# Kernel optimization log

Hardware: AMD Instinct MI355X
Metric: run time of the kernel (lower is better)

## Reference

```python
import jax, jax.numpy as jnp
import numpy as np

NUM_HEADS = 16
D_MODEL = 1024
D_QKV = 64


def _xavier(key, shape):
    # xavier normal over last two dims (fan_in = D_MODEL, fan_out = D_QKV)
    std = float(np.sqrt(2.0 / (shape[-2] + shape[-1])))
    return jax.random.normal(key, shape, dtype=jnp.float32) * std


def setup_inputs() -> dict:
    key = jax.random.key(0)
    ks = jax.random.split(key, 9)
    B, L = 4, 2048
    q = jax.random.normal(ks[0], (B, L, D_MODEL), dtype=jnp.float32)
    k = jax.random.normal(ks[1], (B, L, D_MODEL), dtype=jnp.float32)
    v = jax.random.normal(ks[2], (B, L, D_MODEL), dtype=jnp.float32)
    mask = jax.random.randint(ks[3], (B, L, L), 0, 2, dtype=jnp.int32)
    Wq = _xavier(ks[4], (NUM_HEADS, D_MODEL, D_QKV))
    Wk = _xavier(ks[5], (NUM_HEADS, D_MODEL, D_QKV))
    Wv = _xavier(ks[6], (NUM_HEADS, D_MODEL, D_QKV))
    lim = float(1.0 / np.sqrt(D_MODEL))
    Wo_w = jax.random.uniform(ks[7], (D_MODEL, D_MODEL), minval=-lim, maxval=lim, dtype=jnp.float32)
    Wo_b = jax.random.uniform(ks[8], (D_MODEL,), minval=-lim, maxval=lim, dtype=jnp.float32)
    return {"q": q, "k": k, "v": v, "mask": mask,
            "Wq": Wq, "Wk": Wk, "Wv": Wv, "Wo_w": Wo_w, "Wo_b": Wo_b}


def reference(q, k, v, mask, Wq, Wk, Wv, Wo_w, Wo_b):
    B, L, _ = q.shape
    query = jnp.einsum('blm,nmd->bnld', q, Wq)   # [B,H,L,Dq]
    key_ = jnp.einsum('blm,nmd->bnld', k, Wk)
    value = jnp.einsum('blm,nmd->bnld', v, Wv)
    scores = jnp.einsum('bnld,bnmd->bnlm', query, key_) / jnp.sqrt(
        jnp.asarray(D_QKV, dtype=query.dtype))          # [B,H,L,L]
    scores = jnp.where(mask[:, None, :, :] == 0, jnp.asarray(-1e9, scores.dtype), scores)
    attn = jax.nn.softmax(scores, axis=-1)
    out = jnp.einsum('bnlm,bnmd->bnld', attn, value)     # [B,H,L,Dq]
    out = out.transpose(0, 2, 1, 3).reshape(B, L, D_MODEL)
    return out @ Wo_w.T + Wo_b
```

## Files before the change

kernel.cpp:

```cpp
#include <hip/hip_runtime.h>
#include <stdint.h>

typedef __bf16 bf16;
typedef __bf16 bf16x8 __attribute__((ext_vector_type(8)));
typedef float  f32x4  __attribute__((ext_vector_type(4)));
typedef uint32_t u32;
typedef uint64_t u64;

#define SCALE_L2E 0.18033688011112042f

__device__ __forceinline__ void gld_lds16(const void* gsrc, void* ldst) {
  __builtin_amdgcn_global_load_lds(
      (const __attribute__((address_space(1))) void*)gsrc,
      (__attribute__((address_space(3))) void*)ldst, 16, 0, 0);
}

__global__ void prep(const float* __restrict__ q, const float* __restrict__ k,
                     const float* __restrict__ v, const int* __restrict__ mask,
                     const float* __restrict__ Wq, const float* __restrict__ Wk,
                     const float* __restrict__ Wv, const float* __restrict__ Wo,
                     bf16* __restrict__ qkv, bf16* __restrict__ Wt, u32* __restrict__ mbits) {
  __shared__ float lds[64][65];
  const int z = blockIdx.z;
  const int t = threadIdx.x;
  const int tg = blockIdx.x * 256 + t;
  if (z < 3) {
    const float* in = (z == 0) ? q : (z == 1) ? k : v;
    bf16* o = qkv + (size_t)z * 8388608;
#pragma unroll
    for (int it = 0; it < 2; ++it) {
      int i = tg + it * 524288;
      const float4* p = (const float4*)(in + (size_t)i * 8);
      float4 a = p[0], b = p[1];
      bf16x8 vv;
      vv[0]=(bf16)a.x; vv[1]=(bf16)a.y; vv[2]=(bf16)a.z; vv[3]=(bf16)a.w;
      vv[4]=(bf16)b.x; vv[5]=(bf16)b.y; vv[6]=(bf16)b.z; vv[7]=(bf16)b.w;
      *(bf16x8*)(o + (size_t)i * 8) = vv;
    }
  } else if (z == 3) {
    const int blk = blockIdx.x;
    if (blk < 768) {
      int s = blk >> 8, sub = blk & 255;
      int h = sub >> 4, mblk = sub & 15;
      const float* W = (s == 0) ? Wq : (s == 1) ? Wk : Wv;
      const float* src = W + h * 65536 + mblk * 4096;
#pragma unroll
      for (int i = 0; i < 16; ++i) {
        int idx = t + i * 256;
        lds[idx >> 6][idx & 63] = src[idx];
      }
      __syncthreads();
      int d = t >> 2, o0 = t & 3;
#pragma unroll
      for (int oo = 0; oo < 2; ++oo) {
        int o = o0 + oo * 4;
        bf16x8 vv;
#pragma unroll
        for (int j = 0; j < 8; ++j)
          vv[j] = (bf16)lds[o * 8 + j][d];
        *(bf16x8*)&Wt[(size_t)s * 1048576 + (size_t)(h * 64 + d) * 1024 + mblk * 64 + o * 8] = vv;
      }
    } else if (blk < 832) {
      int idx0 = (blk - 768) * 256 + t;
      for (int i = idx0; i < 131072; i += 16384) {
        const float4* p = (const float4*)&Wo[i * 8];
        float4 a = p[0], b = p[1];
        bf16x8 vv;
        vv[0]=(bf16)a.x; vv[1]=(bf16)a.y; vv[2]=(bf16)a.z; vv[3]=(bf16)a.w;
        vv[4]=(bf16)b.x; vv[5]=(bf16)b.y; vv[6]=(bf16)b.z; vv[7]=(bf16)b.w;
        *(bf16x8*)&Wt[3145728 + (size_t)i * 8] = vv;
      }
    }
  } else {
    for (int idx = tg; idx < 16777216; idx += 524288) {
      int m = mask[idx];
      u64 bal = __ballot(m != 0);
      if ((t & 63) == 0)
        *(u64*)&mbits[idx >> 5] = bal;
    }
  }
}

#define GEMM_CORE(Ap_, Bp_)                                                    \
  __shared__ bf16 sA[2][4096];                                                 \
  __shared__ bf16 sB[2][4096];                                                 \
  const int tid = threadIdx.x;                                                 \
  const int lane = tid & 63, w = tid >> 6;                                     \
  const int c = lane & 15, g = lane >> 4;                                      \
  const int wr = w >> 1, wc = w & 1;                                           \
  const int rr0 = tid >> 3, p0 = tid & 7;                                      \
  const int l0 = p0 ^ (rr0 & 7);                                               \
  const size_t so0 = (size_t)(2 * rr0 + (l0 >> 2)) * 1024 + (l0 & 3) * 8;      \
  const int rr1 = (256 + tid) >> 3, p1 = tid & 7;                              \
  const int l1 = p1 ^ (rr1 & 7);                                               \
  const size_t so1 = (size_t)(2 * rr1 + (l1 >> 2)) * 1024 + (l1 & 3) * 8;      \
  const bf16* As0 = (Ap_) + so0;                                               \
  const bf16* As1 = (Ap_) + so1;                                               \
  const bf16* Bs0 = (Bp_) + so0;                                               \
  const bf16* Bs1 = (Bp_) + so1;                                               \
  const int fro = (c >> 1) * 128 + ((((c & 1) * 4 + g) ^ (c >> 1)) << 4);      \
  const int abase = wr * 4096 + fro;                                           \
  const int bbase = wc * 4096 + fro;                                           \
  f32x4 acc[4][4] = {};                                                        \
  gld_lds16(As0, (char*)&sA[0][0] + tid * 16);                                 \
  gld_lds16(As1, (char*)&sA[0][0] + 4096 + tid * 16);                          \
  gld_lds16(Bs0, (char*)&sB[0][0] + tid * 16);                                 \
  gld_lds16(Bs1, (char*)&sB[0][0] + 4096 + tid * 16);                          \
  for (int k0 = 0; k0 < 1024; k0 += 32) {                                      \
    __syncthreads();                                                           \
    int cb = (k0 >> 5) & 1, nb = cb ^ 1;                                       \
    if (k0 < 992) {                                                            \
      gld_lds16(As0 + k0 + 32, (char*)&sA[nb][0] + tid * 16);                  \
      gld_lds16(As1 + k0 + 32, (char*)&sA[nb][0] + 4096 + tid * 16);           \
      gld_lds16(Bs0 + k0 + 32, (char*)&sB[nb][0] + tid * 16);                  \
      gld_lds16(Bs1 + k0 + 32, (char*)&sB[nb][0] + 4096 + tid * 16);           \
    }                                                                          \
    const char* a8 = (const char*)&sA[cb][0] + abase;                          \
    const char* b8 = (const char*)&sB[cb][0] + bbase;                          \
    bf16x8 af[4], bfr[4];                                                      \
    _Pragma("unroll")                                                          \
    for (int m = 0; m < 4; ++m)                                                \
      af[m] = *(const bf16x8*)(a8 + m * 1024);                                 \
    _Pragma("unroll")                                                          \
    for (int n = 0; n < 4; ++n)                                                \
      bfr[n] = *(const bf16x8*)(b8 + n * 1024);                                \
    _Pragma("unroll")                                                          \
    for (int m = 0; m < 4; ++m)                                                \
      _Pragma("unroll")                                                        \
      for (int n = 0; n < 4; ++n)                                              \
        acc[m][n] = __builtin_amdgcn_mfma_f32_16x16x32_bf16(af[m], bfr[n], acc[m][n], 0, 0, 0); \
  }

__global__ __launch_bounds__(256, 4)
void proj_fused(const bf16* __restrict__ qkv, const bf16* __restrict__ Wt,
                bf16* __restrict__ Qp, bf16* __restrict__ Kp, bf16* __restrict__ Vt) {
  const int wg = blockIdx.x;
  const bf16* Ap;
  const bf16* Bp;
  int row0, col0, stage;
  if (wg < 1024) {
    int swz = (wg & 7) * 128 + (wg >> 3);
    int bx = swz & 7, by = swz >> 3;
    row0 = by * 128; col0 = bx * 128;
    stage = (row0 >= 8192) ? 1 : 0;
    Ap = qkv + (size_t)row0 * 1024;
    Bp = Wt + (stage ? 1048576 : 0) + (size_t)col0 * 1024;
  } else {
    int w2 = wg - 1024;
    int bz = w2 >> 7, rem = w2 & 127;
    int swz = (rem & 7) * 16 + (rem >> 3);
    int bx = swz & 15, by = swz >> 4;
    row0 = by * 128; col0 = bx * 128;
    stage = 2 + bz;
    Ap = Wt + 2097152 + (size_t)row0 * 1024;
    Bp = qkv + 16777216 + (size_t)bz * 2097152 + (size_t)col0 * 1024;
  }

  GEMM_CORE(Ap, Bp)

  if (stage <= 1) {
    float csc = stage ? 1.0f : SCALE_L2E;
    bf16* dst = stage ? Kp : Qp;
#pragma unroll
    for (int m = 0; m < 4; ++m) {
      int row_base = (row0 & 8191) + wr * 64 + m * 16 + g * 4;
#pragma unroll
      for (int n = 0; n < 4; ++n) {
        int col = col0 + wc * 64 + n * 16 + c;
#pragma unroll
        for (int r = 0; r < 4; ++r) {
          int row = row_base + r;
          int b = row >> 11, l = row & 2047, h = col >> 6, d = col & 63;
          dst[(((size_t)(b * 16 + h) * 2048 + l) << 6) + d] = (bf16)(acc[m][n][r] * csc);
        }
      }
    }
  } else {
    int bz = stage - 2;
#pragma unroll
    for (int m = 0; m < 4; ++m) {
      int row_base = row0 + wr * 64 + m * 16 + g * 4;
#pragma unroll
      for (int n = 0; n < 4; ++n) {
        int col = col0 + wc * 64 + n * 16 + c;
#pragma unroll
        for (int r = 0; r < 4; ++r)
          Vt[((size_t)(bz * 1024 + row_base + r)) * 2048 + col] = (bf16)acc[m][n][r];
      }
    }
  }
}

__global__ __launch_bounds__(256, 4)
void gemm_out(const bf16* __restrict__ X, const bf16* __restrict__ Wot,
              float* __restrict__ out, const float* __restrict__ bias) {
  int lin = blockIdx.y * 8 + blockIdx.x;
  int swz = (lin & 7) * 64 + (lin >> 3);
  int bx = swz & 7, by = swz >> 3;
  const int row0 = by * 128, col0 = bx * 128;
  const bf16* Ap = X + (size_t)row0 * 1024;
  const bf16* Bp = Wot + (size_t)col0 * 1024;

  GEMM_CORE(Ap, Bp)

#pragma unroll
  for (int m = 0; m < 4; ++m) {
    int row_base = row0 + wr * 64 + m * 16 + g * 4;
#pragma unroll
    for (int n = 0; n < 4; ++n) {
      int col = col0 + wc * 64 + n * 16 + c;
#pragma unroll
      for (int r = 0; r < 4; ++r)
        out[(size_t)(row_base + r) * 1024 + col] = acc[m][n][r] + bias[col];
    }
  }
}

__global__ __launch_bounds__(256, 4)
void attn_fwd(const bf16* __restrict__ Qp, const bf16* __restrict__ Kp,
              const bf16* __restrict__ Vt, const u32* __restrict__ mbits,
              bf16* __restrict__ X) {
  int lin = blockIdx.y * 16 + blockIdx.x;
  int swz = (lin & 7) * 128 + (lin >> 3);
  int qt = swz & 15, bh = swz >> 4;
  int b = bh >> 4, h = bh & 15;
  int q0 = qt * 128;

  const int tid = threadIdx.x;
  const int lane = tid & 63, w = tid >> 6;
  const int c = lane & 15, g = lane >> 4;

  __shared__ char smem[24576];
  char* sKV = smem;
  char* sPw = smem + 16384 + w * 2048;

  const int c7 = c & 7;
  const int ko0 = c * 128 + ((g ^ c7) << 4);
  const int ko1 = c * 128 + (((4 + g) ^ c7) << 4);
  const int pr_off = (c >> 1) * 128 + ((((c & 1) * 4 + g) ^ (c >> 1)) << 4);
  int pwo[2];
#pragma unroll
  for (int nk = 0; nk < 2; ++nk)
    pwo[nk] = (c >> 1) * 128 + ((((c & 1) * 4 + nk * 2 + (g >> 1)) ^ (c >> 1)) << 4) + (g & 1) * 8;

  const int kr_ = tid >> 3, kb_ = tid & 7;
  const int dK = kr_ * 128 + ((kb_ ^ (kr_ & 7)) << 4);
  const int vd_ = tid >> 2, vk_ = tid & 3;
  const int dV = 4096 + (vd_ >> 1) * 128 + (((((vd_ & 1) << 2) + vk_) ^ ((vd_ >> 1) & 7)) << 4);
  const bf16* gK = Kp + (size_t)bh * 131072 + kr_ * 64 + kb_ * 8;
  const bf16* gV = Vt + ((size_t)(b * 1024 + h * 64 + vd_)) * 2048 + vk_ * 8;

  const bf16* Qbase = Qp + ((size_t)bh * 2048) * 64;
  bf16x8 qf[2][2];
#pragma unroll
  for (int nq = 0; nq < 2; ++nq) {
    int qg = q0 + w * 32 + nq * 16 + c;
#pragma unroll
    for (int kk = 0; kk < 2; ++kk)
      qf[nq][kk] = *(const bf16x8*)&Qbase[(size_t)qg * 64 + kk * 32 + g * 8];
  }

  bf16x8 onesv;
#pragma unroll
  for (int i = 0; i < 8; ++i) onesv[i] = (bf16)1.0f;

  const u32* Mrow0 = mbits + ((size_t)b * 2048 + (q0 + w * 32 + c)) * 64;
  const u32* Mrow1 = mbits + ((size_t)b * 2048 + (q0 + w * 32 + 16 + c)) * 64;

  f32x4 oacc[4][2] = {};
  f32x4 dacc[2] = {};

  {
    uint4 kr = *(const uint4*)gK;
    uint4 vr = *(const uint4*)gV;
    *(uint4*)(sKV + dK) = kr;
    *(uint4*)(sKV + dV) = vr;
  }
  u32 mw0 = Mrow0[0], mw1 = Mrow1[0];

  for (int t = 0; t < 64; ++t) {
    __syncthreads();
    const char* kbuf = sKV + ((t & 1) << 13);

    uint4 kr, vr;
    u32 mn0 = 0, mn1 = 0;
    if (t < 63) {
      kr = *(const uint4*)(gK + (size_t)(t + 1) * 2048);
      vr = *(const uint4*)(gV + (size_t)(t + 1) * 32);
      mn0 = Mrow0[t + 1];
      mn1 = Mrow1[t + 1];
    }

    f32x4 st[2][2] = {};
    __builtin_amdgcn_s_setprio(1);
#pragma unroll
    for (int nk = 0; nk < 2; ++nk) {
      bf16x8 kfa = *(const bf16x8*)(kbuf + ko0 + nk * 2048);
      st[nk][0] = __builtin_amdgcn_mfma_f32_16x16x32_bf16(kfa, qf[0][0], st[nk][0], 0, 0, 0);
      st[nk][1] = __builtin_amdgcn_mfma_f32_16x16x32_bf16(kfa, qf[1][0], st[nk][1], 0, 0, 0);
      bf16x8 kfb = *(const bf16x8*)(kbuf + ko1 + nk * 2048);
      st[nk][0] = __builtin_amdgcn_mfma_f32_16x16x32_bf16(kfb, qf[0][1], st[nk][0], 0, 0, 0);
      st[nk][1] = __builtin_amdgcn_mfma_f32_16x16x32_bf16(kfb, qf[1][1], st[nk][1], 0, 0, 0);
    }
    __builtin_amdgcn_s_setprio(0);

#pragma unroll
    for (int nq = 0; nq < 2; ++nq) {
      u32 ms = (nq ? mw1 : mw0) >> (4 * g);
#pragma unroll
      for (int nk = 0; nk < 2; ++nk) {
        const int bs = nk * 16;
        float e0 = __builtin_amdgcn_exp2f(st[nk][nq][0]);
        float e1 = __builtin_amdgcn_exp2f(st[nk][nq][1]);
        float e2 = __builtin_amdgcn_exp2f(st[nk][nq][2]);
        float e3 = __builtin_amdgcn_exp2f(st[nk][nq][3]);
        e0 = (ms & (1u << (bs + 0))) ? e0 : 0.f;
        e1 = (ms & (1u << (bs + 1))) ? e1 : 0.f;
        e2 = (ms & (1u << (bs + 2))) ? e2 : 0.f;
        e3 = (ms & (1u << (bs + 3))) ? e3 : 0.f;
        union { bf16 hh[4]; uint2 dd; } pk;
        pk.hh[0] = (bf16)e0; pk.hh[1] = (bf16)e1;
        pk.hh[2] = (bf16)e2; pk.hh[3] = (bf16)e3;
        *(uint2*)(sPw + pwo[nk] + nq * 1024) = pk.dd;
      }
    }

    __builtin_amdgcn_s_setprio(1);
    {
      bf16x8 pf0 = *(const bf16x8*)(sPw + pr_off);
      bf16x8 pf1 = *(const bf16x8*)(sPw + pr_off + 1024);
      dacc[0] = __builtin_amdgcn_mfma_f32_16x16x32_bf16(onesv, pf0, dacc[0], 0, 0, 0);
      dacc[1] = __builtin_amdgcn_mfma_f32_16x16x32_bf16(onesv, pf1, dacc[1], 0, 0, 0);
#pragma unroll
      for (int md = 0; md < 4; ++md) {
        bf16x8 vf = *(const bf16x8*)(kbuf + 4096 + pr_off + md * 1024);
        oacc[md][0] = __builtin_amdgcn_mfma_f32_16x16x32_bf16(vf, pf0, oacc[md][0], 0, 0, 0);
        oacc[md][1] = __builtin_amdgcn_mfma_f32_16x16x32_bf16(vf, pf1, oacc[md][1], 0, 0, 0);
      }
    }
    __builtin_amdgcn_s_setprio(0);

    if (t < 63) {
      char* nbuf = sKV + (((t + 1) & 1) << 13);
      *(uint4*)(nbuf + dK) = kr;
      *(uint4*)(nbuf + dV) = vr;
    }
    mw0 = mn0; mw1 = mn1;
  }

  float inv0 = 1.f / dacc[0][0];
  float inv1 = 1.f / dacc[1][0];

  __syncthreads();
  char* Xl = smem;
#pragma unroll
  for (int nq = 0; nq < 2; ++nq) {
    float inv = nq ? inv1 : inv0;
    int ql = w * 32 + nq * 16 + c;
#pragma unroll
    for (int md = 0; md < 4; ++md)
#pragma unroll
      for (int r = 0; r < 4; ++r) {
        int d = md * 16 + g * 4 + r;
        int blk = d >> 3, off = d & 7;
        *(bf16*)(Xl + ql * 128 + ((blk ^ (ql & 7)) << 4) + off * 2) =
            (bf16)(oacc[md][nq][r] * inv);
      }
  }
  __syncthreads();
#pragma unroll
  for (int i = 0; i < 4; ++i) {
    int u = i * 256 + tid;
    int row = u >> 3, blk = u & 7;
    uint4 xv = *(const uint4*)(Xl + row * 128 + ((blk ^ (row & 7)) << 4));
    *(uint4*)&X[(size_t)(b * 2048 + q0 + row) * 1024 + h * 64 + blk * 8] = xv;
  }
}


extern "C" void kernel_launch(void* const* d_in, const int* in_sizes, int n_in,
                              void* d_out, int out_size, void* d_ws, size_t ws_size,
                              hipStream_t stream) {
  const float* q    = (const float*)d_in[0];
  const float* k    = (const float*)d_in[1];
  const float* v    = (const float*)d_in[2];
  const int*   mask = (const int*)d_in[3];
  const float* Wq   = (const float*)d_in[4];
  const float* Wk   = (const float*)d_in[5];
  const float* Wv   = (const float*)d_in[6];
  const float* Wo   = (const float*)d_in[7];
  const float* Wb   = (const float*)d_in[8];

  char* ws = (char*)d_ws;
  bf16* qkv = (bf16*)(ws + 0);
  bf16* Wt  = (bf16*)(ws + 50331648);
  bf16* Qp  = (bf16*)(ws + 58720256);
  bf16* Kp  = (bf16*)(ws + 75497472);
  bf16* Vt  = (bf16*)(ws + 92274688);
  bf16* Xb  = (bf16*)(ws + 109051904);
  u32*  mb  = (u32*) (ws + 125829120);

  prep<<<dim3(2048, 1, 5), 256, 0, stream>>>(q, k, v, mask, Wq, Wk, Wv, Wo, qkv, Wt, mb);

  proj_fused<<<dim3(1536, 1, 1), 256, 0, stream>>>(qkv, Wt, Qp, Kp, Vt);

  attn_fwd<<<dim3(16, 64, 1), 256, 0, stream>>>(Qp, Kp, Vt, mb, Xb);

  gemm_out<<<dim3(8, 64, 1), 256, 0, stream>>>(Xb, Wt + 3145728, (float*)d_out, Wb);
}
```

Measured before the change: 247.5 us.

## Fuse fp32-to-bf16 input conversion into projection GEMM tile loads

Drops the separate pass that converted q/k/v activations to a bf16 workspace. The projection GEMM now loads fp32 tiles straight into registers, converts them, and writes packed bf16 into LDS, with the write placed after the MFMA block as a register-staged prefetch. This saves a full fp32 read plus a bf16 write and re-read of 48M elements. In exchange the fused path reads fp32 tiles again per column tile (about 8x reuse) and loses the async global-to-LDS path for the fp32 operand, which adds register pressure. The prep kernel is also flattened and the bias load is hoisted out of the inner loop.

```diff
diff --git a/kernel.cpp b/kernel.cpp
--- a/kernel.cpp
+++ b/kernel.cpp
@@ -15,63 +15,53 @@
       (__attribute__((address_space(3))) void*)ldst, 16, 0, 0);
 }
 
-__global__ void prep(const float* __restrict__ q, const float* __restrict__ k,
-                     const float* __restrict__ v, const int* __restrict__ mask,
+__device__ __forceinline__ void pack_wr(float4 x0, float4 x1, void* dst) {
+  bf16x8 vv;
+  vv[0]=(bf16)x0.x; vv[1]=(bf16)x0.y; vv[2]=(bf16)x0.z; vv[3]=(bf16)x0.w;
+  vv[4]=(bf16)x1.x; vv[5]=(bf16)x1.y; vv[6]=(bf16)x1.z; vv[7]=(bf16)x1.w;
+  *(bf16x8*)dst = vv;
+}
+
+__global__ void prep(const int* __restrict__ mask,
                      const float* __restrict__ Wq, const float* __restrict__ Wk,
                      const float* __restrict__ Wv, const float* __restrict__ Wo,
-                     bf16* __restrict__ qkv, bf16* __restrict__ Wt, u32* __restrict__ mbits) {
+                     bf16* __restrict__ Wt, u32* __restrict__ mbits) {
   __shared__ float lds[64][65];
-  const int z = blockIdx.z;
+  const int blk = blockIdx.x;
   const int t = threadIdx.x;
-  const int tg = blockIdx.x * 256 + t;
-  if (z < 3) {
-    const float* in = (z == 0) ? q : (z == 1) ? k : v;
-    bf16* o = qkv + (size_t)z * 8388608;
-#pragma unroll
-    for (int it = 0; it < 2; ++it) {
-      int i = tg + it * 524288;
-      const float4* p = (const float4*)(in + (size_t)i * 8);
+  if (blk < 768) {
+    int s = blk >> 8, sub = blk & 255;
+    int h = sub >> 4, mblk = sub & 15;
+    const float* W = (s == 0) ? Wq : (s == 1) ? Wk : Wv;
+    const float* src = W + h * 65536 + mblk * 4096;
+#pragma unroll
+    for (int i = 0; i < 16; ++i) {
+      int idx = t + i * 256;
+      lds[idx >> 6][idx & 63] = src[idx];
+    }
+    __syncthreads();
+    int d = t >> 2, o0 = t & 3;
+#pragma unroll
+    for (int oo = 0; oo < 2; ++oo) {
+      int o = o0 + oo * 4;
+      bf16x8 vv;
+#pragma unroll
+      for (int j = 0; j < 8; ++j)
+        vv[j] = (bf16)lds[o * 8 + j][d];
+      *(bf16x8*)&Wt[(size_t)s * 1048576 + (size_t)(h * 64 + d) * 1024 + mblk * 64 + o * 8] = vv;
+    }
+  } else if (blk < 832) {
+    int idx0 = (blk - 768) * 256 + t;
+    for (int i = idx0; i < 131072; i += 16384) {
+      const float4* p = (const float4*)&Wo[i * 8];
       float4 a = p[0], b = p[1];
       bf16x8 vv;
       vv[0]=(bf16)a.x; vv[1]=(bf16)a.y; vv[2]=(bf16)a.z; vv[3]=(bf16)a.w;
       vv[4]=(bf16)b.x; vv[5]=(bf16)b.y; vv[6]=(bf16)b.z; vv[7]=(bf16)b.w;
-      *(bf16x8*)(o + (size_t)i * 8) = vv;
-    }
-  } else if (z == 3) {
-    const int blk = blockIdx.x;
-    if (blk < 768) {
-      int s = blk >> 8, sub = blk & 255;
-      int h = sub >> 4, mblk = sub & 15;
-      const float* W = (s == 0) ? Wq : (s == 1) ? Wk : Wv;
-      const float* src = W + h * 65536 + mblk * 4096;
-#pragma unroll
-      for (int i = 0; i < 16; ++i) {
-        int idx = t + i * 256;
-        lds[idx >> 6][idx & 63] = src[idx];
-      }
-      __syncthreads();
-      int d = t >> 2, o0 = t & 3;
-#pragma unroll
-      for (int oo = 0; oo < 2; ++oo) {
-        int o = o0 + oo * 4;
-        bf16x8 vv;
-#pragma unroll
-        for (int j = 0; j < 8; ++j)
-          vv[j] = (bf16)lds[o * 8 + j][d];
-        *(bf16x8*)&Wt[(size_t)s * 1048576 + (size_t)(h * 64 + d) * 1024 + mblk * 64 + o * 8] = vv;
-      }
-    } else if (blk < 832) {
-      int idx0 = (blk - 768) * 256 + t;
-      for (int i = idx0; i < 131072; i += 16384) {
-        const float4* p = (const float4*)&Wo[i * 8];
-        float4 a = p[0], b = p[1];
-        bf16x8 vv;
-        vv[0]=(bf16)a.x; vv[1]=(bf16)a.y; vv[2]=(bf16)a.z; vv[3]=(bf16)a.w;
-        vv[4]=(bf16)b.x; vv[5]=(bf16)b.y; vv[6]=(bf16)b.z; vv[7]=(bf16)b.w;
-        *(bf16x8*)&Wt[3145728 + (size_t)i * 8] = vv;
-      }
+      *(bf16x8*)&Wt[3145728 + (size_t)i * 8] = vv;
     }
   } else {
+    int tg = (blk - 832) * 256 + t;
     for (int idx = tg; idx < 16777216; idx += 524288) {
       int m = mask[idx];
       u64 bal = __ballot(m != 0);
@@ -81,102 +71,151 @@
   }
 }
 
-#define GEMM_CORE(Ap_, Bp_)                                                    \
-  __shared__ bf16 sA[2][4096];                                                 \
-  __shared__ bf16 sB[2][4096];                                                 \
-  const int tid = threadIdx.x;                                                 \
-  const int lane = tid & 63, w = tid >> 6;                                     \
-  const int c = lane & 15, g = lane >> 4;                                      \
-  const int wr = w >> 1, wc = w & 1;                                           \
-  const int rr0 = tid >> 3, p0 = tid & 7;                                      \
-  const int l0 = p0 ^ (rr0 & 7);                                               \
-  const size_t so0 = (size_t)(2 * rr0 + (l0 >> 2)) * 1024 + (l0 & 3) * 8;      \
-  const int rr1 = (256 + tid) >> 3, p1 = tid & 7;                              \
-  const int l1 = p1 ^ (rr1 & 7);                                               \
-  const size_t so1 = (size_t)(2 * rr1 + (l1 >> 2)) * 1024 + (l1 & 3) * 8;      \
-  const bf16* As0 = (Ap_) + so0;                                               \
-  const bf16* As1 = (Ap_) + so1;                                               \
-  const bf16* Bs0 = (Bp_) + so0;                                               \
-  const bf16* Bs1 = (Bp_) + so1;                                               \
-  const int fro = (c >> 1) * 128 + ((((c & 1) * 4 + g) ^ (c >> 1)) << 4);      \
-  const int abase = wr * 4096 + fro;                                           \
-  const int bbase = wc * 4096 + fro;                                           \
-  f32x4 acc[4][4] = {};                                                        \
-  gld_lds16(As0, (char*)&sA[0][0] + tid * 16);                                 \
-  gld_lds16(As1, (char*)&sA[0][0] + 4096 + tid * 16);                          \
-  gld_lds16(Bs0, (char*)&sB[0][0] + tid * 16);                                 \
-  gld_lds16(Bs1, (char*)&sB[0][0] + 4096 + tid * 16);                          \
-  for (int k0 = 0; k0 < 1024; k0 += 32) {                                      \
-    __syncthreads();                                                           \
-    int cb = (k0 >> 5) & 1, nb = cb ^ 1;                                       \
-    if (k0 < 992) {                                                            \
-      gld_lds16(As0 + k0 + 32, (char*)&sA[nb][0] + tid * 16);                  \
-      gld_lds16(As1 + k0 + 32, (char*)&sA[nb][0] + 4096 + tid * 16);           \
-      gld_lds16(Bs0 + k0 + 32, (char*)&sB[nb][0] + tid * 16);                  \
-      gld_lds16(Bs1 + k0 + 32, (char*)&sB[nb][0] + 4096 + tid * 16);           \
-    }                                                                          \
-    const char* a8 = (const char*)&sA[cb][0] + abase;                          \
-    const char* b8 = (const char*)&sB[cb][0] + bbase;                          \
-    bf16x8 af[4], bfr[4];                                                      \
-    _Pragma("unroll")                                                          \
-    for (int m = 0; m < 4; ++m)                                                \
-      af[m] = *(const bf16x8*)(a8 + m * 1024);                                 \
-    _Pragma("unroll")                                                          \
-    for (int n = 0; n < 4; ++n)                                                \
-      bfr[n] = *(const bf16x8*)(b8 + n * 1024);                                \
-    _Pragma("unroll")                                                          \
-    for (int m = 0; m < 4; ++m)                                                \
-      _Pragma("unroll")                                                        \
-      for (int n = 0; n < 4; ++n)                                              \
-        acc[m][n] = __builtin_amdgcn_mfma_f32_16x16x32_bf16(af[m], bfr[n], acc[m][n], 0, 0, 0); \
-  }
+template<bool AF, bool BF>
+__device__ __forceinline__ void gemm_core(
+    const float* Af, const bf16* Ab,
+    const float* Bf, const bf16* Bb,
+    bf16 (&sA)[2][4096], bf16 (&sB)[2][4096],
+    f32x4 (&acc)[4][4])
+{
+  const int tid = threadIdx.x;
+  const int lane = tid & 63, w = tid >> 6;
+  const int c = lane & 15, g = lane >> 4;
+  const int wr = w >> 1, wc = w & 1;
+
+  const int rr0 = tid >> 3;
+  const int l0 = (tid & 7) ^ (rr0 & 7);
+  const size_t soA0 = (size_t)(2 * rr0 + (l0 >> 2)) * 1024 + (l0 & 3) * 8;
+  const size_t soA1 = soA0 + (size_t)64 * 1024;
+
+  const int fro = (c >> 1) * 128 + ((((c & 1) * 4 + g) ^ (c >> 1)) << 4);
+  const int abase = wr * 4096 + fro;
+  const int bbase = wc * 4096 + fro;
+
+  char* dA0 = (char*)&sA[0][0];
+  char* dB0 = (char*)&sB[0][0];
+
+  if constexpr (AF) {
+    pack_wr(*(const float4*)(Af + soA0), *(const float4*)(Af + soA0 + 4), dA0 + tid * 16);
+    pack_wr(*(const float4*)(Af + soA1), *(const float4*)(Af + soA1 + 4), dA0 + 4096 + tid * 16);
+  } else {
+    gld_lds16(Ab + soA0, dA0 + tid * 16);
+    gld_lds16(Ab + soA1, dA0 + 4096 + tid * 16);
+  }
+  if constexpr (BF) {
+    pack_wr(*(const float4*)(Bf + soA0), *(const float4*)(Bf + soA0 + 4), dB0 + tid * 16);
+    pack_wr(*(const float4*)(Bf + soA1), *(const float4*)(Bf + soA1 + 4), dB0 + 4096 + tid * 16);
+  } else {
+    gld_lds16(Bb + soA0, dB0 + tid * 16);
+    gld_lds16(Bb + soA1, dB0 + 4096 + tid * 16);
+  }
+
+  for (int k0 = 0; k0 < 1024; k0 += 32) {
+    __syncthreads();
+    const int cb = (k0 >> 5) & 1, nb = cb ^ 1;
+    char* dAn = (char*)&sA[nb][0];
+    char* dBn = (char*)&sB[nb][0];
+
+    float4 ra0, ra1, ra2, ra3, rb0, rb1, rb2, rb3;
+    if (k0 < 992) {
+      if constexpr (AF) {
+        ra0 = *(const float4*)(Af + soA0 + k0 + 32);
+        ra1 = *(const float4*)(Af + soA0 + k0 + 36);
+        ra2 = *(const float4*)(Af + soA1 + k0 + 32);
+        ra3 = *(const float4*)(Af + soA1 + k0 + 36);
+      } else {
+        gld_lds16(Ab + soA0 + k0 + 32, dAn + tid * 16);
+        gld_lds16(Ab + soA1 + k0 + 32, dAn + 4096 + tid * 16);
+      }
+      if constexpr (BF) {
+        rb0 = *(const float4*)(Bf + soA0 + k0 + 32);
+        rb1 = *(const float4*)(Bf + soA0 + k0 + 36);
+        rb2 = *(const float4*)(Bf + soA1 + k0 + 32);
+        rb3 = *(const float4*)(Bf + soA1 + k0 + 36);
+      } else {
+        gld_lds16(Bb + soA0 + k0 + 32, dBn + tid * 16);
+        gld_lds16(Bb + soA1 + k0 + 32, dBn + 4096 + tid * 16);
+      }
+    }
+
+    const char* a8 = (const char*)&sA[cb][0] + abase;
+    const char* b8 = (const char*)&sB[cb][0] + bbase;
+    bf16x8 af[4], bfr[4];
+#pragma unroll
+    for (int m = 0; m < 4; ++m)
+      af[m] = *(const bf16x8*)(a8 + m * 1024);
+#pragma unroll
+    for (int n = 0; n < 4; ++n)
+      bfr[n] = *(const bf16x8*)(b8 + n * 1024);
+#pragma unroll
+    for (int m = 0; m < 4; ++m)
+#pragma unroll
+      for (int n = 0; n < 4; ++n)
+        acc[m][n] = __builtin_amdgcn_mfma_f32_16x16x32_bf16(af[m], bfr[n], acc[m][n], 0, 0, 0);
+
+    if (k0 < 992) {
+      if constexpr (AF) {
+        pack_wr(ra0, ra1, dAn + tid * 16);
+        pack_wr(ra2, ra3, dAn + 4096 + tid * 16);
+      }
+      if constexpr (BF) {
+        pack_wr(rb0, rb1, dBn + tid * 16);
+        pack_wr(rb2, rb3, dBn + 4096 + tid * 16);
+      }
+    }
+  }
+}
 
 __global__ __launch_bounds__(256, 4)
-void proj_fused(const bf16* __restrict__ qkv, const bf16* __restrict__ Wt,
+void proj_fused(const float* __restrict__ q, const float* __restrict__ k,
+                const float* __restrict__ v, const bf16* __restrict__ Wt,
                 bf16* __restrict__ Qp, bf16* __restrict__ Kp, bf16* __restrict__ Vt) {
+  __shared__ bf16 sA[2][4096];
+  __shared__ bf16 sB[2][4096];
   const int wg = blockIdx.x;
-  const bf16* Ap;
-  const bf16* Bp;
-  int row0, col0, stage;
+  const int lane = threadIdx.x & 63, w = threadIdx.x >> 6;
+  const int c = lane & 15, g = lane >> 4;
+  const int wr = w >> 1, wc = w & 1;
+  f32x4 acc[4][4] = {};
+
   if (wg < 1024) {
     int swz = (wg & 7) * 128 + (wg >> 3);
     int bx = swz & 7, by = swz >> 3;
-    row0 = by * 128; col0 = bx * 128;
-    stage = (row0 >= 8192) ? 1 : 0;
-    Ap = qkv + (size_t)row0 * 1024;
-    Bp = Wt + (stage ? 1048576 : 0) + (size_t)col0 * 1024;
+    const int row0 = by * 128, col0 = bx * 128;
+    const int isK = (row0 >= 8192);
+    const float* Af = isK ? (k + (size_t)(row0 - 8192) * 1024)
+                          : (q + (size_t)row0 * 1024);
+    const bf16* Bb = Wt + (isK ? 1048576 : 0) + (size_t)col0 * 1024;
+
+    gemm_core<true, false>(Af, nullptr, nullptr, Bb, sA, sB, acc);
+
+    float csc = isK ? 1.0f : SCALE_L2E;
+    bf16* dst = isK ? Kp : Qp;
+#pragma unroll
+    for (int m = 0; m < 4; ++m) {
+      int row_base = (row0 & 8191) + wr * 64 + m * 16 + g * 4;
+#pragma unroll
+      for (int n = 0; n < 4; ++n) {
+        int col = col0 + wc * 64 + n * 16 + c;
+#pragma unroll
+        for (int r = 0; r < 4; ++r) {
+          int row = row_base + r;
+          int b = row >> 11, l = row & 2047, h = col >> 6, d = col & 63;
+          dst[(((size_t)(b * 16 + h) * 2048 + l) << 6) + d] = (bf16)(acc[m][n][r] * csc);
+        }
+      }
+    }
   } else {
     int w2 = wg - 1024;
     int bz = w2 >> 7, rem = w2 & 127;
     int swz = (rem & 7) * 16 + (rem >> 3);
     int bx = swz & 15, by = swz >> 4;
-    row0 = by * 128; col0 = bx * 128;
-    stage = 2 + bz;
-    Ap = Wt + 2097152 + (size_t)row0 * 1024;
-    Bp = qkv + 16777216 + (size_t)bz * 2097152 + (size_t)col0 * 1024;
-  }
-
-  GEMM_CORE(Ap, Bp)
-
-  if (stage <= 1) {
-    float csc = stage ? 1.0f : SCALE_L2E;
-    bf16* dst = stage ? Kp : Qp;
-#pragma unroll
-    for (int m = 0; m < 4; ++m) {
-      int row_base = (row0 & 8191) + wr * 64 + m * 16 + g * 4;
-#pragma unroll
-      for (int n = 0; n < 4; ++n) {
-        int col = col0 + wc * 64 + n * 16 + c;
-#pragma unroll
-        for (int r = 0; r < 4; ++r) {
-          int row = row_base + r;
-          int b = row >> 11, l = row & 2047, h = col >> 6, d = col & 63;
-          dst[(((size_t)(b * 16 + h) * 2048 + l) << 6) + d] = (bf16)(acc[m][n][r] * csc);
-        }
-      }
-    }
-  } else {
-    int bz = stage - 2;
+    const int row0 = by * 128, col0 = bx * 128;
+    const bf16* Ab = Wt + 2097152 + (size_t)row0 * 1024;
+    const float* Bf = v + (size_t)bz * 2097152 + (size_t)col0 * 1024;
+
+    gemm_core<false, true>(nullptr, Ab, Bf, nullptr, sA, sB, acc);
+
 #pragma unroll
     for (int m = 0; m < 4; ++m) {
       int row_base = row0 + wr * 64 + m * 16 + g * 4;
@@ -194,14 +233,19 @@
 __global__ __launch_bounds__(256, 4)
 void gemm_out(const bf16* __restrict__ X, const bf16* __restrict__ Wot,
               float* __restrict__ out, const float* __restrict__ bias) {
+  __shared__ bf16 sA[2][4096];
+  __shared__ bf16 sB[2][4096];
   int lin = blockIdx.y * 8 + blockIdx.x;
   int swz = (lin & 7) * 64 + (lin >> 3);
   int bx = swz & 7, by = swz >> 3;
   const int row0 = by * 128, col0 = bx * 128;
-  const bf16* Ap = X + (size_t)row0 * 1024;
-  const bf16* Bp = Wot + (size_t)col0 * 1024;
-
-  GEMM_CORE(Ap, Bp)
+  const int lane = threadIdx.x & 63, w = threadIdx.x >> 6;
+  const int c = lane & 15, g = lane >> 4;
+  const int wr = w >> 1, wc = w & 1;
+  f32x4 acc[4][4] = {};
+
+  gemm_core<false, false>(nullptr, X + (size_t)row0 * 1024,
+                          nullptr, Wot + (size_t)col0 * 1024, sA, sB, acc);
 
 #pragma unroll
   for (int m = 0; m < 4; ++m) {
@@ -209,9 +253,10 @@
 #pragma unroll
     for (int n = 0; n < 4; ++n) {
       int col = col0 + wc * 64 + n * 16 + c;
+      float bv = bias[col];
 #pragma unroll
       for (int r = 0; r < 4; ++r)
-        out[(size_t)(row_base + r) * 1024 + col] = acc[m][n][r] + bias[col];
+        out[(size_t)(row_base + r) * 1024 + col] = acc[m][n][r] + bv;
     }
   }
 }
@@ -392,7 +437,6 @@
   const float* Wb   = (const float*)d_in[8];
 
   char* ws = (char*)d_ws;
-  bf16* qkv = (bf16*)(ws + 0);
   bf16* Wt  = (bf16*)(ws + 50331648);
   bf16* Qp  = (bf16*)(ws + 58720256);
   bf16* Kp  = (bf16*)(ws + 75497472);
@@ -400,9 +444,9 @@
   bf16* Xb  = (bf16*)(ws + 109051904);
   u32*  mb  = (u32*) (ws + 125829120);
 
-  prep<<<dim3(2048, 1, 5), 256, 0, stream>>>(q, k, v, mask, Wq, Wk, Wv, Wo, qkv, Wt, mb);
-
-  proj_fused<<<dim3(1536, 1, 1), 256, 0, stream>>>(qkv, Wt, Qp, Kp, Vt);
+  prep<<<dim3(2880, 1, 1), 256, 0, stream>>>(mask, Wq, Wk, Wv, Wo, Wt, mb);
+
+  proj_fused<<<dim3(1536, 1, 1), 256, 0, stream>>>(q, k, v, Wt, Qp, Kp, Vt);
 
   attn_fwd<<<dim3(16, 64, 1), 256, 0, stream>>>(Qp, Kp, Vt, mb, Xb);
 
```

After: 267.8 us. 1.08x slower.
